# Kernel optimization log

Hardware: AMD Instinct MI355X
Metric: run time of the kernel (lower is better)

## Reference

```python
import jax, jax.numpy as jnp
import numpy as np

GRID = (32, 16, 8)      # grid_resolution [nx, ny, nz]
RADIUS = 0.25           # ball-query radius
K = 10                  # neighbors_in_radius (max neighbors returned)


def setup_inputs() -> dict:
    key = jax.random.key(0)
    k1, k2 = jax.random.split(key)
    B, N = 1, 32768
    nx, ny, nz = GRID
    x = jax.random.uniform(k1, (B, N, 3), dtype=jnp.float32)
    p_grid = jax.random.uniform(k2, (B, nx, ny, nz, 3), dtype=jnp.float32)
    return {"x": x, "p_grid": p_grid}


def _ball_query(db, q):
    """For each query point, return indices + coords of up to K database points
    within RADIUS (first-K in index order; invalid slots -> index 0, coords 0).
    db: (B, G, 3) database points; q: (B, N, 3) query points.
    """
    G = db.shape[1]
    # squared pairwise distances (B, N, G) -- the dense reference for the
    # hash-grid accelerated warp kernel
    d2 = jnp.sum((q[:, :, None, :] - db[:, None, :, :]) ** 2, axis=-1)
    mask = d2 <= jnp.asarray(RADIUS * RADIUS, d2.dtype)
    # prefer lowest database index among in-radius points: score G-i if valid
    score = jnp.where(mask, (G - jnp.arange(G, dtype=jnp.int32))[None, None, :], 0)
    vals, idx = jax.lax.top_k(score, K)            # (B, N, K)
    valid = vals > 0
    mapping = jnp.where(valid, idx, 0)             # (B, N, K) int32
    gathered = jax.vmap(lambda d, m: d[m])(db, mapping)  # (B, N, K, 3)
    outputs = gathered * valid[..., None].astype(db.dtype)
    return mapping, outputs


def reference(x, p_grid):
    # BQWarp.forward with reverse_mapping=True:
    #   database = flattened p_grid, queries = x coords
    B = x.shape[0]
    nx, ny, nz = GRID
    grid = jnp.reshape(p_grid, (B, nx * ny * nz, 3))
    mapping, outputs = _ball_query(grid, x[..., :3])
    return mapping, outputs
```

## Files before the change

kernel.cpp:

```cpp
#include <hip/hip_runtime.h>


#define BQ_K 10
#define BQ_R2 0.0625f

__global__ __launch_bounds__(256) void bqwarp_ballot_kernel(
    const float* __restrict__ x,
    const float* __restrict__ db,
    float* __restrict__ out_map,
    float* __restrict__ out_pts,
    int N, int G)
{
    const int lane = threadIdx.x & 63;
    const int wave = threadIdx.x >> 6;
    const int q = blockIdx.x * 4 + wave;
    if (q >= N) return;

    const float qx = x[3 * q + 0];
    const float qy = x[3 * q + 1];
    const float qz = x[3 * q + 2];

    float* __restrict__ omap = out_map + (size_t)q * BQ_K;
    float* __restrict__ opts = out_pts + (size_t)q * BQ_K * 3;

    const unsigned long long below = (1ull << lane) - 1ull;

    int cnt = 0;
    const int nchunk = (G + 63) >> 6;

    for (int c = 0; c < nchunk; ++c) {
        const int gi = (c << 6) | lane;
        const int gil = gi < G ? gi : G - 1;
        const float px = db[3 * gil + 0];
        const float py = db[3 * gil + 1];
        const float pz = db[3 * gil + 2];
        const float dx = __fsub_rn(qx, px);
        const float dy = __fsub_rn(qy, py);
        const float dz = __fsub_rn(qz, pz);
        const float d2 = __fadd_rn(
            __fadd_rn(__fmul_rn(dx, dx), __fmul_rn(dy, dy)),
            __fmul_rn(dz, dz));
        const bool hit = (gi < G) && (d2 <= BQ_R2);

        const unsigned long long m = __ballot(hit);
        if (hit) {
            const int slot = cnt + __popcll(m & below);
            if (slot < BQ_K) {
                omap[slot] = (float)gi;
                opts[3 * slot + 0] = px;
                opts[3 * slot + 1] = py;
                opts[3 * slot + 2] = pz;
            }
        }
        cnt += __popcll(m);
        if (cnt >= BQ_K) break;
    }

    const int c0 = cnt < BQ_K ? cnt : BQ_K;
    if (lane >= c0 && lane < BQ_K) {
        omap[lane] = 0.0f;
        opts[3 * lane + 0] = 0.0f;
        opts[3 * lane + 1] = 0.0f;
        opts[3 * lane + 2] = 0.0f;
    }
}

extern "C" void kernel_launch(void* const* d_in, const int* in_sizes, int n_in,
                              void* d_out, int out_size, void* d_ws, size_t ws_size,
                              hipStream_t stream) {
    const float* x  = (const float*)d_in[0];
    const float* pg = (const float*)d_in[1];

    const int N = in_sizes[0] / 3;
    const int G = in_sizes[1] / 3;

    float* out_map = (float*)d_out;
    float* out_pts = out_map + (size_t)N * BQ_K;

    const int block = 256;
    const int nblk = (N + 3) / 4;
    bqwarp_ballot_kernel<<<nblk, block, 0, stream>>>(x, pg, out_map, out_pts, N, G);
}
```

Before: 68.40 us.

## Repack grid points into padded float4 workspace and prefetch next chunk

Adds a small pre-pass that repacks the grid database into 16-byte float4 entries padded to a multiple of 64, with far-away sentinel points in the padding. The query kernel then does one vector load per point instead of three scalar loads, drops the bounds check, and software-prefetches the next chunk's point while testing the current one. This costs an extra kernel launch and workspace traffic, and the prefetch adds register pressure and a possibly wasted load after an early exit.

```diff
diff --git a/kernel.cpp b/kernel.cpp
--- a/kernel.cpp
+++ b/kernel.cpp
@@ -4,12 +4,25 @@
 #define BQ_K 10
 #define BQ_R2 0.0625f
 
-__global__ __launch_bounds__(256) void bqwarp_ballot_kernel(
+__global__ __launch_bounds__(256) void bq_repack_kernel(
+    const float* __restrict__ db, float4* __restrict__ db4, int G, int Gpad)
+{
+    const int i = blockIdx.x * 256 + threadIdx.x;
+    if (i < Gpad) {
+        if (i < G) {
+            db4[i] = make_float4(db[3 * i + 0], db[3 * i + 1], db[3 * i + 2], 0.0f);
+        } else {
+            db4[i] = make_float4(1e30f, 1e30f, 1e30f, 0.0f);
+        }
+    }
+}
+
+__global__ __launch_bounds__(256) void bqwarp_kernel(
     const float* __restrict__ x,
-    const float* __restrict__ db,
+    const float4* __restrict__ db4,
     float* __restrict__ out_map,
     float* __restrict__ out_pts,
-    int N, int G)
+    int N, int nchunk)
 {
     const int lane = threadIdx.x & 63;
     const int wave = threadIdx.x >> 6;
@@ -26,34 +39,34 @@
     const unsigned long long below = (1ull << lane) - 1ull;
 
     int cnt = 0;
-    const int nchunk = (G + 63) >> 6;
+    float4 p = db4[lane];
 
     for (int c = 0; c < nchunk; ++c) {
-        const int gi = (c << 6) | lane;
-        const int gil = gi < G ? gi : G - 1;
-        const float px = db[3 * gil + 0];
-        const float py = db[3 * gil + 1];
-        const float pz = db[3 * gil + 2];
-        const float dx = __fsub_rn(qx, px);
-        const float dy = __fsub_rn(qy, py);
-        const float dz = __fsub_rn(qz, pz);
+        const int cn = (c + 1 < nchunk) ? c + 1 : c;
+        const float4 pn = db4[(cn << 6) | lane];
+
+        const float dx = __fsub_rn(qx, p.x);
+        const float dy = __fsub_rn(qy, p.y);
+        const float dz = __fsub_rn(qz, p.z);
         const float d2 = __fadd_rn(
             __fadd_rn(__fmul_rn(dx, dx), __fmul_rn(dy, dy)),
             __fmul_rn(dz, dz));
-        const bool hit = (gi < G) && (d2 <= BQ_R2);
+        const bool hit = (d2 <= BQ_R2);
 
         const unsigned long long m = __ballot(hit);
         if (hit) {
             const int slot = cnt + __popcll(m & below);
             if (slot < BQ_K) {
+                const int gi = (c << 6) | lane;
                 omap[slot] = (float)gi;
-                opts[3 * slot + 0] = px;
-                opts[3 * slot + 1] = py;
-                opts[3 * slot + 2] = pz;
+                opts[3 * slot + 0] = p.x;
+                opts[3 * slot + 1] = p.y;
+                opts[3 * slot + 2] = p.z;
             }
         }
         cnt += __popcll(m);
         if (cnt >= BQ_K) break;
+        p = pn;
     }
 
     const int c0 = cnt < BQ_K ? cnt : BQ_K;
@@ -77,7 +90,13 @@
     float* out_map = (float*)d_out;
     float* out_pts = out_map + (size_t)N * BQ_K;
 
+    const int nchunk = (G + 63) >> 6;
+    const int Gpad = nchunk << 6;
+    float4* db4 = (float4*)d_ws;
+
+    bq_repack_kernel<<<(Gpad + 255) / 256, 256, 0, stream>>>(pg, db4, G, Gpad);
+
     const int block = 256;
     const int nblk = (N + 3) / 4;
-    bqwarp_ballot_kernel<<<nblk, block, 0, stream>>>(x, pg, out_map, out_pts, N, G);
+    bqwarp_kernel<<<nblk, block, 0, stream>>>(x, db4, out_map, out_pts, N, nchunk);
 }
```

Result: slower. 69.80 us (+2.0%).

## Process four queries per wave sharing database loads, with register prefetch

Applied to the files above, without the earlier changes.

Each wave now handles four query points at once, so every database chunk loaded from memory is reused for four distance tests. The next chunk's coordinates are prefetched into registers while the current one is processed. Launch bounds now request higher occupancy, and the grid shrinks by a factor of four. The early exit waits until all four queries have K hits, which adds some wasted iterations. The code also assumes N is a multiple of 4 and G a multiple of 64, because the tail guards were dropped.

```diff
diff --git a/kernel.cpp b/kernel.cpp
--- a/kernel.cpp
+++ b/kernel.cpp
@@ -3,8 +3,9 @@
 
 #define BQ_K 10
 #define BQ_R2 0.0625f
+#define NQ 4
 
-__global__ __launch_bounds__(256) void bqwarp_ballot_kernel(
+__global__ __launch_bounds__(256, 8) void bqwarp_kernel(
     const float* __restrict__ x,
     const float* __restrict__ db,
     float* __restrict__ out_map,
@@ -13,55 +14,77 @@
 {
     const int lane = threadIdx.x & 63;
     const int wave = threadIdx.x >> 6;
-    const int q = blockIdx.x * 4 + wave;
-    if (q >= N) return;
+    const int qb = (blockIdx.x * 4 + wave) * NQ;
+    if (qb >= N) return;
 
-    const float qx = x[3 * q + 0];
-    const float qy = x[3 * q + 1];
-    const float qz = x[3 * q + 2];
-
-    float* __restrict__ omap = out_map + (size_t)q * BQ_K;
-    float* __restrict__ opts = out_pts + (size_t)q * BQ_K * 3;
+    float qx[NQ], qy[NQ], qz[NQ];
+    int cnt[NQ];
+#pragma unroll
+    for (int j = 0; j < NQ; ++j) {
+        qx[j] = x[3 * (qb + j) + 0];
+        qy[j] = x[3 * (qb + j) + 1];
+        qz[j] = x[3 * (qb + j) + 2];
+        cnt[j] = 0;
+    }
 
     const unsigned long long below = (1ull << lane) - 1ull;
+    const int nchunk = G >> 6;
 
-    int cnt = 0;
-    const int nchunk = (G + 63) >> 6;
+    float px = db[3 * lane + 0];
+    float py = db[3 * lane + 1];
+    float pz = db[3 * lane + 2];
 
     for (int c = 0; c < nchunk; ++c) {
+        const int cn = (c + 1 < nchunk) ? c + 1 : c;
+        const int gn = (cn << 6) | lane;
+        const float nx = db[3 * gn + 0];
+        const float ny = db[3 * gn + 1];
+        const float nz = db[3 * gn + 2];
+
         const int gi = (c << 6) | lane;
-        const int gil = gi < G ? gi : G - 1;
-        const float px = db[3 * gil + 0];
-        const float py = db[3 * gil + 1];
-        const float pz = db[3 * gil + 2];
-        const float dx = __fsub_rn(qx, px);
-        const float dy = __fsub_rn(qy, py);
-        const float dz = __fsub_rn(qz, pz);
-        const float d2 = __fadd_rn(
-            __fadd_rn(__fmul_rn(dx, dx), __fmul_rn(dy, dy)),
-            __fmul_rn(dz, dz));
-        const bool hit = (gi < G) && (d2 <= BQ_R2);
 
-        const unsigned long long m = __ballot(hit);
-        if (hit) {
-            const int slot = cnt + __popcll(m & below);
-            if (slot < BQ_K) {
-                omap[slot] = (float)gi;
-                opts[3 * slot + 0] = px;
-                opts[3 * slot + 1] = py;
-                opts[3 * slot + 2] = pz;
+#pragma unroll
+        for (int j = 0; j < NQ; ++j) {
+            const float dx = __fsub_rn(qx[j], px);
+            const float dy = __fsub_rn(qy[j], py);
+            const float dz = __fsub_rn(qz[j], pz);
+            const float d2 = __fadd_rn(
+                __fadd_rn(__fmul_rn(dx, dx), __fmul_rn(dy, dy)),
+                __fmul_rn(dz, dz));
+            const bool hit = (d2 <= BQ_R2);
+            const unsigned long long m = __ballot(hit);
+            if (hit) {
+                const int slot = cnt[j] + __popcll(m & below);
+                if (slot < BQ_K) {
+                    float* omap = out_map + (size_t)(qb + j) * BQ_K;
+                    float* opts = out_pts + (size_t)(qb + j) * BQ_K * 3;
+                    omap[slot] = (float)gi;
+                    opts[3 * slot + 0] = px;
+                    opts[3 * slot + 1] = py;
+                    opts[3 * slot + 2] = pz;
+                }
             }
+            cnt[j] += __popcll(m);
         }
-        cnt += __popcll(m);
-        if (cnt >= BQ_K) break;
+
+        if (cnt[0] >= BQ_K && cnt[1] >= BQ_K &&
+            cnt[2] >= BQ_K && cnt[3] >= BQ_K) break;
+
+        px = nx; py = ny; pz = nz;
     }
 
-    const int c0 = cnt < BQ_K ? cnt : BQ_K;
-    if (lane >= c0 && lane < BQ_K) {
-        omap[lane] = 0.0f;
-        opts[3 * lane + 0] = 0.0f;
-        opts[3 * lane + 1] = 0.0f;
-        opts[3 * lane + 2] = 0.0f;
+#pragma unroll
+    for (int j = 0; j < NQ; ++j) {
+        const int s = lane - 16 * j;
+        const int c0 = cnt[j] < BQ_K ? cnt[j] : BQ_K;
+        if (s >= c0 && s < BQ_K) {
+            float* omap = out_map + (size_t)(qb + j) * BQ_K;
+            float* opts = out_pts + (size_t)(qb + j) * BQ_K * 3;
+            omap[s] = 0.0f;
+            opts[3 * s + 0] = 0.0f;
+            opts[3 * s + 1] = 0.0f;
+            opts[3 * s + 2] = 0.0f;
+        }
     }
 }
 
@@ -78,6 +101,6 @@
     float* out_pts = out_map + (size_t)N * BQ_K;
 
     const int block = 256;
-    const int nblk = (N + 3) / 4;
-    bqwarp_ballot_kernel<<<nblk, block, 0, stream>>>(x, pg, out_map, out_pts, N, G);
+    const int nblk = (N + 16 - 1) / 16;
+    bqwarp_kernel<<<nblk, block, 0, stream>>>(x, pg, out_map, out_pts, N, G);
 }
```

Result: no change. 68.10 us (-0.4%).

## Software-pipeline database loads two chunks ahead and process chunks in pairs

Applied to the files above, without the earlier changes.

Restructures the per-query scan so each wave handles two 64-point chunks per iteration, prefetching the next pair of database points into registers while it evaluates the current pair. This hides global load latency on the serial chunk loop. It also drops the bounds checks, replaces the popcount prefix with mbcnt, and adds an occupancy hint to launch_bounds. The cost is that G must be a multiple of 128 (it is 4096 here), and the early exit now happens only every two chunks, so some extra work is done past the point where K hits are found.

```diff
diff --git a/kernel.cpp b/kernel.cpp
--- a/kernel.cpp
+++ b/kernel.cpp
@@ -4,7 +4,7 @@
 #define BQ_K 10
 #define BQ_R2 0.0625f
 
-__global__ __launch_bounds__(256) void bqwarp_ballot_kernel(
+__global__ __launch_bounds__(256, 8) void bqwarp_kernel(
     const float* __restrict__ x,
     const float* __restrict__ db,
     float* __restrict__ out_map,
@@ -23,37 +23,80 @@
     float* __restrict__ omap = out_map + (size_t)q * BQ_K;
     float* __restrict__ opts = out_pts + (size_t)q * BQ_K * 3;
 
-    const unsigned long long below = (1ull << lane) - 1ull;
+    const int nchunk = G >> 6;
+    int cnt = 0;
 
-    int cnt = 0;
-    const int nchunk = (G + 63) >> 6;
+    float ax = db[3 * lane + 0];
+    float ay = db[3 * lane + 1];
+    float az = db[3 * lane + 2];
+    float bx = db[3 * (64 + lane) + 0];
+    float by = db[3 * (64 + lane) + 1];
+    float bz = db[3 * (64 + lane) + 2];
 
-    for (int c = 0; c < nchunk; ++c) {
-        const int gi = (c << 6) | lane;
-        const int gil = gi < G ? gi : G - 1;
-        const float px = db[3 * gil + 0];
-        const float py = db[3 * gil + 1];
-        const float pz = db[3 * gil + 2];
-        const float dx = __fsub_rn(qx, px);
-        const float dy = __fsub_rn(qy, py);
-        const float dz = __fsub_rn(qz, pz);
-        const float d2 = __fadd_rn(
-            __fadd_rn(__fmul_rn(dx, dx), __fmul_rn(dy, dy)),
-            __fmul_rn(dz, dz));
-        const bool hit = (gi < G) && (d2 <= BQ_R2);
+    for (int c = 0; c < nchunk; c += 2) {
+        const int cA = (c + 2 < nchunk) ? c + 2 : c;
+        const int cB = (c + 3 < nchunk) ? c + 3 : c + 1;
+        const int gA = (cA << 6) | lane;
+        const int gB = (cB << 6) | lane;
+        const float nax = db[3 * gA + 0];
+        const float nay = db[3 * gA + 1];
+        const float naz = db[3 * gA + 2];
+        const float nbx = db[3 * gB + 0];
+        const float nby = db[3 * gB + 1];
+        const float nbz = db[3 * gB + 2];
 
-        const unsigned long long m = __ballot(hit);
-        if (hit) {
-            const int slot = cnt + __popcll(m & below);
-            if (slot < BQ_K) {
-                omap[slot] = (float)gi;
-                opts[3 * slot + 0] = px;
-                opts[3 * slot + 1] = py;
-                opts[3 * slot + 2] = pz;
+        {
+            const float dx = __fsub_rn(qx, ax);
+            const float dy = __fsub_rn(qy, ay);
+            const float dz = __fsub_rn(qz, az);
+            const float d2 = __fadd_rn(
+                __fadd_rn(__fmul_rn(dx, dx), __fmul_rn(dy, dy)),
+                __fmul_rn(dz, dz));
+            const bool hit = (d2 <= BQ_R2);
+            const unsigned long long m = __ballot(hit);
+            if (hit) {
+                const int prefix = __builtin_amdgcn_mbcnt_hi(
+                    (unsigned)(m >> 32),
+                    __builtin_amdgcn_mbcnt_lo((unsigned)m, 0u));
+                const int slot = cnt + prefix;
+                if (slot < BQ_K) {
+                    omap[slot] = (float)((c << 6) | lane);
+                    opts[3 * slot + 0] = ax;
+                    opts[3 * slot + 1] = ay;
+                    opts[3 * slot + 2] = az;
+                }
             }
+            cnt += __popcll(m);
         }
-        cnt += __popcll(m);
+
+        {
+            const float dx = __fsub_rn(qx, bx);
+            const float dy = __fsub_rn(qy, by);
+            const float dz = __fsub_rn(qz, bz);
+            const float d2 = __fadd_rn(
+                __fadd_rn(__fmul_rn(dx, dx), __fmul_rn(dy, dy)),
+                __fmul_rn(dz, dz));
+            const bool hit = (d2 <= BQ_R2);
+            const unsigned long long m = __ballot(hit);
+            if (hit) {
+                const int prefix = __builtin_amdgcn_mbcnt_hi(
+                    (unsigned)(m >> 32),
+                    __builtin_amdgcn_mbcnt_lo((unsigned)m, 0u));
+                const int slot = cnt + prefix;
+                if (slot < BQ_K) {
+                    omap[slot] = (float)(((c + 1) << 6) | lane);
+                    opts[3 * slot + 0] = bx;
+                    opts[3 * slot + 1] = by;
+                    opts[3 * slot + 2] = bz;
+                }
+            }
+            cnt += __popcll(m);
+        }
+
         if (cnt >= BQ_K) break;
+
+        ax = nax; ay = nay; az = naz;
+        bx = nbx; by = nby; bz = nbz;
     }
 
     const int c0 = cnt < BQ_K ? cnt : BQ_K;
@@ -79,5 +122,5 @@
 
     const int block = 256;
     const int nblk = (N + 3) / 4;
-    bqwarp_ballot_kernel<<<nblk, block, 0, stream>>>(x, pg, out_map, out_pts, N, G);
+    bqwarp_kernel<<<nblk, block, 0, stream>>>(x, pg, out_map, out_pts, N, G);
 }
```

Result: no change. 68.77 us (+0.5%).
